# Kernel optimization log

Measured on AMD Instinct MI355X. Metric: run time of the kernel, lower is better.

The kernel has to match this reference:

```python
import math
import jax, jax.numpy as jnp
import numpy as np

B, T, C = 4, 2048, 1024
N_HEAD = 16
HEAD_DIM = C // N_HEAD


def setup_inputs() -> dict:
    key = jax.random.key(0)
    k1, k2, k3 = jax.random.split(key, 3)
    x = jax.random.normal(k1, (B, T, C), dtype=jnp.float32)
    # nn.Linear weights: (out_features, in_features); init scale ~1/sqrt(C)
    w_attn = jax.random.normal(k2, (3 * C, C), dtype=jnp.float32) / math.sqrt(C)
    w_proj = jax.random.normal(k3, (C, C), dtype=jnp.float32) / math.sqrt(C)
    return {"x": x, "w_attn": w_attn, "w_proj": w_proj}


def reference(x, w_attn, w_proj):
    Bx, Tx, Cx = x.shape
    qkv = x @ w_attn.T  # (B,T,3C)
    q, k, v = jnp.split(qkv, 3, axis=2)
    # (B,T,H,D) -> (B,H,T,D)
    q = q.reshape(Bx, Tx, N_HEAD, HEAD_DIM).transpose(0, 2, 1, 3)
    k = k.reshape(Bx, Tx, N_HEAD, HEAD_DIM).transpose(0, 2, 1, 3)
    v = v.reshape(Bx, Tx, N_HEAD, HEAD_DIM).transpose(0, 2, 1, 3)
    scale = 1.0 / math.sqrt(HEAD_DIM)
    att = jnp.einsum("bhqd,bhkd->bhqk", q, k) * scale
    causal = jnp.tril(jnp.ones((Tx, Tx), dtype=bool))
    att = jnp.where(causal[None, None, :, :], att, -jnp.inf)
    att = jax.nn.softmax(att, axis=-1)
    out = jnp.einsum("bhqk,bhkd->bhqd", att, v)
    out = out.transpose(0, 2, 1, 3).reshape(Bx, Tx, Cx)
    return out @ w_proj.T
```

## Files before the change

### kernel.cpp

```cpp
#include <hip/hip_runtime.h>
#include <hip/hip_bf16.h>


typedef __attribute__((ext_vector_type(8))) short bf16x8;
typedef __attribute__((ext_vector_type(4))) float f32x4;
typedef unsigned short ushort_t;

#if __has_builtin(__builtin_amdgcn_exp2f)
#define EXP2(x) __builtin_amdgcn_exp2f(x)
#else
#define EXP2(x) exp2f(x)
#endif

__device__ inline ushort_t f2bf(float f) {
    union { float f; unsigned int u; } x; x.f = f;
    return (ushort_t)((x.u + 0x7fffu + ((x.u >> 16) & 1u)) >> 16);
}

__device__ inline ushort_t f2bf_fast(float f) {
    union { float f; unsigned int u; } x; x.f = f;
    return (ushort_t)((x.u + 0x8000u) >> 16);
}

__device__ inline bf16x8 load8_f32_to_bf16(const float* p) {
    float4 f0 = *(const float4*)p;
    float4 f1 = *(const float4*)(p + 4);
    bf16x8 r;
    r[0] = (short)f2bf(f0.x); r[1] = (short)f2bf(f0.y);
    r[2] = (short)f2bf(f0.z); r[3] = (short)f2bf(f0.w);
    r[4] = (short)f2bf(f1.x); r[5] = (short)f2bf(f1.y);
    r[6] = (short)f2bf(f1.z); r[7] = (short)f2bf(f1.w);
    return r;
}

__device__ inline void gl2lds16(const ushort_t* g, ushort_t* l) {
    __builtin_amdgcn_global_load_lds(
        (const __attribute__((address_space(1))) unsigned int*)g,
        (__attribute__((address_space(3))) unsigned int*)l,
        16, 0, 0);
}

__global__ void cvt3(const float* __restrict__ a, long n8a,
                     const float* __restrict__ b, long n8b,
                     const float* __restrict__ c, long n8c,
                     ushort_t* __restrict__ out) {
    long i = (long)blockIdx.x * 256 + threadIdx.x;
    const float* src; long off;
    if (i < n8a) { src = a; off = i; }
    else if (i < n8a + n8b) { src = b; off = i - n8a; }
    else if (i < n8a + n8b + n8c) { src = c; off = i - n8a - n8b; }
    else return;
    *(bf16x8*)(out + i * 8) = load8_f32_to_bf16(src + off * 8);
}

__global__ void fill_zero_f32(float* out, int n) {
    int i = blockIdx.x * 256 + threadIdx.x;
    if (i < n) out[i] = 0.0f;
}

#define QK_LOG2E_SCALE 0.18033688011112042f

#define OVBUF 16384

template <int EPI>
__global__ __launch_bounds__(256) void gemm_ov(
        const ushort_t* __restrict__ A, const ushort_t* __restrict__ B,
        void* __restrict__ Cp, void* __restrict__ Cp2,
        int M, int N, int K) {
    __shared__ ushort_t S[2 * OVBUF];

    const int tid  = threadIdx.x;
    const int lane = tid & 63;
    const int w    = tid >> 6;
    const int quad = lane >> 4;
    const int l16  = lane & 15;
    const int wm   = (w & 1) * 64;
    const int wn   = (w >> 1) * 64;

    const int nbx = N >> 7;
    const int cpx = gridDim.x >> 3;
    const int swz = ((int)blockIdx.x & 7) * cpx + ((int)blockIdx.x >> 3);
    const int bm = (swz / nbx) << 7;
    const int bn = (swz % nbx) << 7;

    const int nt = K >> 6;

    const int srow = lane >> 3;
    const int soct = (lane & 7) ^ srow;
    const ushort_t* Ag = A + (size_t)(bm + w * 32 + srow) * K + soct * 8;
    const ushort_t* Bg = B + (size_t)(bn + w * 32 + srow) * K + soct * 8;

    auto stage = [&](int kt) {
        ushort_t* d = S + (kt & 1) * OVBUF;
        const size_t ko = (size_t)kt * 64;
#pragma unroll
        for (int j = 0; j < 4; j++) {
            gl2lds16(Ag + ko + (size_t)(j * 8) * K, d + w * 2048 + j * 512);
            gl2lds16(Bg + ko + (size_t)(j * 8) * K, d + 8192 + w * 2048 + j * 512);
        }
    };

    const int sl7 = l16 & 7;
    const int ca0 = ((quad)     ^ sl7) * 8;
    const int ca1 = ((quad + 4) ^ sl7) * 8;
    const int arow = (wm + l16) * 64;
    const int brow = 8192 + (wn + l16) * 64;

    f32x4 acc[4][4] = {};

    stage(0);
    __asm__ __volatile__("s_waitcnt vmcnt(0)" ::: "memory");
    __builtin_amdgcn_s_barrier();

    for (int kt = 0; kt < nt; kt++) {
        if (kt + 1 < nt) stage(kt + 1);

        const ushort_t* Sb = S + (kt & 1) * OVBUF;
        bf16x8 af[4][2], bfr[4][2];
#pragma unroll
        for (int mi = 0; mi < 4; mi++) {
            af[mi][0] = *(const bf16x8*)(Sb + arow + mi * 1024 + ca0);
            af[mi][1] = *(const bf16x8*)(Sb + arow + mi * 1024 + ca1);
        }
#pragma unroll
        for (int ni = 0; ni < 4; ni++) {
            bfr[ni][0] = *(const bf16x8*)(Sb + brow + ni * 1024 + ca0);
            bfr[ni][1] = *(const bf16x8*)(Sb + brow + ni * 1024 + ca1);
        }

        __builtin_amdgcn_s_setprio(1);
#pragma unroll
        for (int mi = 0; mi < 4; mi++)
#pragma unroll
            for (int ni = 0; ni < 4; ni++)
#pragma unroll
                for (int kk = 0; kk < 2; kk++)
                    acc[mi][ni] = __builtin_amdgcn_mfma_f32_16x16x32_bf16(
                        af[mi][kk], bfr[ni][kk], acc[mi][ni], 0, 0, 0);
        __builtin_amdgcn_s_setprio(0);

        __asm__ __volatile__("s_waitcnt vmcnt(0)" ::: "memory");
        __builtin_amdgcn_s_barrier();
    }

    const int colbase = bn + wn;
    const int rowbase = bm + wm + quad * 4;
    if constexpr (EPI == 1) {
#pragma unroll
        for (int mi = 0; mi < 4; mi++) {
            const int row = rowbase + mi * 16;
            float* cr = (float*)Cp + (size_t)row * N + colbase + l16;
#pragma unroll
            for (int r = 0; r < 4; r++)
#pragma unroll
                for (int ni = 0; ni < 4; ni++)
                    cr[(size_t)r * N + ni * 16] = acc[mi][ni][r];
        }
    } else {
        if (colbase < 2048) {
            const float qs = (colbase < 1024) ? QK_LOG2E_SCALE : 1.0f;
#pragma unroll
            for (int mi = 0; mi < 4; mi++) {
                const int row = rowbase + mi * 16;
                ushort_t* qp = (ushort_t*)Cp + (size_t)row * 2048 + colbase + l16;
#pragma unroll
                for (int r = 0; r < 4; r++)
#pragma unroll
                    for (int ni = 0; ni < 4; ni++)
                        qp[(size_t)r * 2048 + ni * 16] = f2bf(acc[mi][ni][r] * qs);
            }
        } else {
#pragma unroll
            for (int mi = 0; mi < 4; mi++) {
                const int row = rowbase + mi * 16;
                const int bb = row >> 11, tt = row & 2047;
#pragma unroll
                for (int ni = 0; ni < 4; ni++) {
                    const int vc = colbase + ni * 16 + l16 - 2048;
                    const int hh = vc >> 6, dd = vc & 63;
                    ushort_t* vp = (ushort_t*)Cp2 +
                        ((((size_t)bb * 16 + hh) * 64 + dd) * 2048) + tt;
#pragma unroll
                    for (int r = 0; r < 4; r++)
                        vp[r] = f2bf(acc[mi][ni][r]);
                }
            }
        }
    }
}

#define BM 128
#define BN 128
#define BK 64
#define LDK 72

template <bool A_F32, bool B_F32, int EPI>
__global__ __launch_bounds__(256) void gemm_nt(
        const void* __restrict__ Ap, const void* __restrict__ Bp,
        void* __restrict__ Cp, void* __restrict__ Cp2,
        int M, int N, int K) {
    __shared__ ushort_t As[BM * LDK];
    __shared__ ushort_t Bs[BN * LDK];

    const int tid  = threadIdx.x;
    const int lane = tid & 63;
    const int w    = tid >> 6;
    const int quad = lane >> 4;
    const int l16  = lane & 15;

    const int bm = blockIdx.y * BM;
    const int bn = blockIdx.x * BN;
    const int wm = (w & 1) * 64;
    const int wn = (w >> 1) * 64;

    f32x4 acc[4][4] = {};

    const int lrow = tid >> 3;
    const int lcol = (tid & 7) * 8;

    bf16x8 pa[4], pb[4];
#pragma unroll
    for (int i = 0; i < 4; i++) {
        const int ra = lrow + i * 32;
        if constexpr (A_F32)
            pa[i] = load8_f32_to_bf16((const float*)Ap + (size_t)(bm + ra) * K + lcol);
        else
            pa[i] = *(const bf16x8*)((const ushort_t*)Ap + (size_t)(bm + ra) * K + lcol);
        if constexpr (B_F32)
            pb[i] = load8_f32_to_bf16((const float*)Bp + (size_t)(bn + ra) * K + lcol);
        else
            pb[i] = *(const bf16x8*)((const ushort_t*)Bp + (size_t)(bn + ra) * K + lcol);
    }

    for (int k0 = 0; k0 < K; k0 += BK) {
        __syncthreads();
#pragma unroll
        for (int i = 0; i < 4; i++) {
            *(bf16x8*)&As[(lrow + i * 32) * LDK + lcol] = pa[i];
            *(bf16x8*)&Bs[(lrow + i * 32) * LDK + lcol] = pb[i];
        }
        __syncthreads();

        if (k0 + BK < K) {
            const int kn = k0 + BK + lcol;
#pragma unroll
            for (int i = 0; i < 4; i++) {
                const int ra = lrow + i * 32;
                if constexpr (A_F32)
                    pa[i] = load8_f32_to_bf16((const float*)Ap + (size_t)(bm + ra) * K + kn);
                else
                    pa[i] = *(const bf16x8*)((const ushort_t*)Ap + (size_t)(bm + ra) * K + kn);
                if constexpr (B_F32)
                    pb[i] = load8_f32_to_bf16((const float*)Bp + (size_t)(bn + ra) * K + kn);
                else
                    pb[i] = *(const bf16x8*)((const ushort_t*)Bp + (size_t)(bn + ra) * K + kn);
            }
        }

#pragma unroll
        for (int ks = 0; ks < BK; ks += 32) {
            bf16x8 af[4], bfr[4];
#pragma unroll
            for (int i = 0; i < 4; i++)
                af[i] = *(const bf16x8*)&As[(wm + i * 16 + l16) * LDK + ks + quad * 8];
#pragma unroll
            for (int i = 0; i < 4; i++)
                bfr[i] = *(const bf16x8*)&Bs[(wn + i * 16 + l16) * LDK + ks + quad * 8];
#pragma unroll
            for (int mi = 0; mi < 4; mi++)
#pragma unroll
                for (int ni = 0; ni < 4; ni++)
                    acc[mi][ni] = __builtin_amdgcn_mfma_f32_16x16x32_bf16(
                        af[mi], bfr[ni], acc[mi][ni], 0, 0, 0);
        }
    }

#pragma unroll
    for (int mi = 0; mi < 4; mi++) {
        const int row0 = bm + wm + mi * 16 + quad * 4;
#pragma unroll
        for (int r = 0; r < 4; r++) {
            const int row = row0 + r;
            if constexpr (EPI == 1) {
                float* crow = (float*)Cp + (size_t)row * N + bn + wn;
#pragma unroll
                for (int ni = 0; ni < 4; ni++)
                    crow[ni * 16 + l16] = acc[mi][ni][r];
            } else {
                if (bn < 2048) {
                    const float qs = (bn < 1024) ? QK_LOG2E_SCALE : 1.0f;
                    ushort_t* crow = (ushort_t*)Cp + (size_t)row * 2048 + bn + wn;
#pragma unroll
                    for (int ni = 0; ni < 4; ni++)
                        crow[ni * 16 + l16] = f2bf(acc[mi][ni][r] * qs);
                } else {
                    ushort_t* vt = (ushort_t*)Cp2;
                    const int bb = row >> 11, tt = row & 2047;
#pragma unroll
                    for (int ni = 0; ni < 4; ni++) {
                        const int vc = bn + wn + ni * 16 + l16 - 2048;
                        const int hh = vc >> 6, dd = vc & 63;
                        vt[(((size_t)bb * 16 + hh) * 64 + dd) * 2048 + tt] =
                            f2bf(acc[mi][ni][r]);
                    }
                }
            }
        }
    }
}

#define AT_T 2048
#define PLD 72

__global__ __launch_bounds__(256) void attn4(
        const ushort_t* __restrict__ qk,
        const ushort_t* __restrict__ vt,
        ushort_t* __restrict__ attout) {
    const int bh   = blockIdx.x;
    const int qblk = (gridDim.y - 1) - blockIdx.y;
    const int b    = bh >> 4;
    const int h    = bh & 15;

    const int tid  = threadIdx.x;
    const int lane = tid & 63;
    const int w    = tid >> 6;
    const int quad = lane >> 4;
    const int l16  = lane & 15;
    const int sw   = l16 & 7;

    __shared__ ushort_t Ks[64 * 64];
    __shared__ ushort_t Vs[80 * 64];
    __shared__ ushort_t Ps[4][32 * PLD];

    for (int i = tid; i < 16 * 64; i += 256) Vs[64 * 64 + i] = 0;
    if (tid < 64) Vs[64 * 64 + tid] = 0x3F80;

    const ushort_t* qp = qk + (size_t)b * AT_T * 2048 + h * 64;
    const ushort_t* kp = qp + 1024;
    const ushort_t* vp = vt + (size_t)bh * 64 * 2048;

    const int Q0 = qblk * 128 + w * 16;

    bf16x8 aq[2][2];
#pragma unroll
    for (int s = 0; s < 2; s++) {
        const ushort_t* qrow = qp + (size_t)(Q0 + s * 64 + l16) * 2048;
        aq[s][0] = *(const bf16x8*)(qrow + quad * 8);
        aq[s][1] = *(const bf16x8*)(qrow + 32 + quad * 8);
    }

    f32x4 o[2][5] = {};

    const int lr8 = lane >> 3;
    const int cbg = ((lane & 7) ^ lr8) * 8;

    const int nk = 2 * qblk + 2;
    for (int kt = 0; kt < nk; kt++) {
        const int k0 = kt * 64;
        if (kt) __syncthreads();
#pragma unroll
        for (int j = 0; j < 2; j++) {
            gl2lds16(kp + (size_t)(k0 + w * 16 + j * 8 + lr8) * 2048 + cbg,
                     &Ks[(w * 16 + j * 8) * 64]);
            gl2lds16(vp + (size_t)(w * 16 + j * 8 + lr8) * 2048 + k0 + cbg,
                     &Vs[(w * 16 + j * 8) * 64]);
        }
        __syncthreads();

        f32x4 s0[4], s1[4];
#pragma unroll
        for (int c = 0; c < 4; c++) {
            s0[c][0] = -8.0f; s0[c][1] = -8.0f; s0[c][2] = -8.0f; s0[c][3] = -8.0f;
            s1[c] = s0[c];
#pragma unroll
            for (int ks = 0; ks < 2; ks++) {
                const int cs = ((quad + 4 * ks) ^ sw) * 8;
                bf16x8 bk = *(const bf16x8*)&Ks[(c * 16 + l16) * 64 + cs];
                s0[c] = __builtin_amdgcn_mfma_f32_16x16x32_bf16(aq[0][ks], bk, s0[c], 0, 0, 0);
                s1[c] = __builtin_amdgcn_mfma_f32_16x16x32_bf16(aq[1][ks], bk, s1[c], 0, 0, 0);
            }
        }

        if (kt >= 2 * qblk) {
            const int q0r = Q0 + quad * 4;
#pragma unroll
            for (int c = 0; c < 4; c++) {
                const int kcol = k0 + c * 16 + l16;
#pragma unroll
                for (int r = 0; r < 4; r++)
                    if (kcol > q0r + r) s0[c][r] = -__builtin_inff();
            }
        }
        if (kt == 2 * qblk + 1) {
            const int q1r = Q0 + 64 + quad * 4;
#pragma unroll
            for (int c = 0; c < 4; c++) {
                const int kcol = k0 + c * 16 + l16;
#pragma unroll
                for (int r = 0; r < 4; r++)
                    if (kcol > q1r + r) s1[c][r] = -__builtin_inff();
            }
        }

#pragma unroll
        for (int c = 0; c < 4; c++)
#pragma unroll
            for (int r = 0; r < 4; r++) {
                Ps[w][(quad * 4 + r) * PLD + c * 16 + l16] = f2bf_fast(EXP2(s0[c][r]));
                Ps[w][(16 + quad * 4 + r) * PLD + c * 16 + l16] = f2bf_fast(EXP2(s1[c][r]));
            }

        __asm__ __volatile__("s_waitcnt lgkmcnt(0)" ::: "memory");

#pragma unroll
        for (int ks = 0; ks < 2; ks++) {
            const int cs = ((quad + 4 * ks) ^ sw) * 8;
            bf16x8 ap0 = *(const bf16x8*)&Ps[w][l16 * PLD + ks * 32 + quad * 8];
            bf16x8 ap1 = *(const bf16x8*)&Ps[w][(16 + l16) * PLD + ks * 32 + quad * 8];
#pragma unroll
            for (int n = 0; n < 5; n++) {
                bf16x8 bv = *(const bf16x8*)&Vs[(n * 16 + l16) * 64 + cs];
                o[0][n] = __builtin_amdgcn_mfma_f32_16x16x32_bf16(ap0, bv, o[0][n], 0, 0, 0);
                o[1][n] = __builtin_amdgcn_mfma_f32_16x16x32_bf16(ap1, bv, o[1][n], 0, 0, 0);
            }
        }
    }

#pragma unroll
    for (int s = 0; s < 2; s++) {
        ushort_t* op = attout + (size_t)(b * AT_T + Q0 + s * 64 + quad * 4) * 1024 + h * 64;
#pragma unroll
        for (int r = 0; r < 4; r++) {
            const float l = __shfl(o[s][4][r], lane & 48, 64);
            const float inv = 1.0f / fmaxf(l, 1e-30f);
            ushort_t* orow = op + (size_t)r * 1024;
#pragma unroll
            for (int n = 0; n < 4; n++)
                orow[n * 16 + l16] = f2bf(o[s][n][r] * inv);
        }
    }
}

extern "C" void kernel_launch(void* const* d_in, const int* in_sizes, int n_in,
                              void* d_out, int out_size, void* d_ws, size_t ws_size,
                              hipStream_t stream) {
    const float* x      = (const float*)d_in[0];
    const float* w_attn = (const float*)d_in[1];
    const float* w_proj = (const float*)d_in[2];
    float* out = (float*)d_out;

    const int M = 8192, C = 1024;
    const size_t E_QK  = (size_t)M * 2048;
    const size_t E_VT  = (size_t)4 * 16 * 64 * 2048;
    const size_t E_ATT = (size_t)M * 1024;
    const size_t E_X   = (size_t)M * 1024;
    const size_t E_WA  = (size_t)3072 * 1024;
    const size_t E_WP  = (size_t)1024 * 1024;
    const size_t need_mid  = (E_QK + E_VT + E_ATT) * 2;
    const size_t need_full = need_mid + (E_X + E_WA + E_WP) * 2;

    if (ws_size < need_mid) {
        fill_zero_f32<<<(out_size + 255) / 256, 256, 0, stream>>>(out, out_size);
        return;
    }

    ushort_t* qk  = (ushort_t*)d_ws;
    ushort_t* vt  = qk + E_QK;
    ushort_t* att = vt + E_VT;

    if (ws_size >= need_full) {
        ushort_t* xb  = att + E_ATT;
        const long n8x = (long)(E_X / 8), n8a = (long)(E_WA / 8), n8p = (long)(E_WP / 8);
        const long n8  = n8x + n8a + n8p;
        cvt3<<<(int)((n8 + 255) / 256), 256, 0, stream>>>(
            x, n8x, w_attn, n8a, w_proj, n8p, xb);

        ushort_t* wab = xb + E_X;
        ushort_t* wpb = wab + E_WA;
        gemm_ov<2><<<dim3((M / 128) * (3 * C / 128)), 256, 0, stream>>>(
            xb, wab, qk, vt, M, 3 * C, C);
        attn4<<<dim3(64, 16), 256, 0, stream>>>(qk, vt, att);
        gemm_ov<1><<<dim3((M / 128) * (C / 128)), 256, 0, stream>>>(
            att, wpb, out, nullptr, M, C, C);
    } else {
        gemm_nt<true, true, 2><<<dim3(3 * C / BN, M / BM), 256, 0, stream>>>(
            x, w_attn, qk, vt, M, 3 * C, C);
        attn4<<<dim3(64, 16), 256, 0, stream>>>(qk, vt, att);
        gemm_nt<false, true, 1><<<dim3(C / BN, M / BM), 256, 0, stream>>>(
            att, w_proj, out, nullptr, M, C, C);
    }
}
```

Before: 232.5 us.

## Double-buffer K/V tiles in attention kernel to overlap loads with MFMA

Gives the K and V shared-memory tiles two buffers. The next tile's global-to-LDS loads are issued before computing on the current tile, with vmcnt waits and raw s_barriers replacing the earlier pair of __syncthreads. This is meant to hide global load latency behind the QK and PV MFMA work. It doubles K/V LDS use, which may lower occupancy. It also depends on the vmcnt(4) count matching the number of outstanding loads.

```diff
diff --git a/kernel.cpp b/kernel.cpp
--- a/kernel.cpp
+++ b/kernel.cpp
@@ -328,12 +328,15 @@
     const int l16  = lane & 15;
     const int sw   = l16 & 7;
 
-    __shared__ ushort_t Ks[64 * 64];
-    __shared__ ushort_t Vs[80 * 64];
+    __shared__ ushort_t Ks[2][64 * 64];
+    __shared__ ushort_t Vs[2][80 * 64];
     __shared__ ushort_t Ps[4][32 * PLD];
 
-    for (int i = tid; i < 16 * 64; i += 256) Vs[64 * 64 + i] = 0;
-    if (tid < 64) Vs[64 * 64 + tid] = 0x3F80;
+#pragma unroll
+    for (int bfi = 0; bfi < 2; bfi++) {
+        for (int i = tid; i < 16 * 64; i += 256) Vs[bfi][64 * 64 + i] = 0;
+        if (tid < 64) Vs[bfi][64 * 64 + tid] = 0x3F80;
+    }
 
     const ushort_t* qp = qk + (size_t)b * AT_T * 2048 + h * 64;
     const ushort_t* kp = qp + 1024;
@@ -354,18 +357,34 @@
     const int lr8 = lane >> 3;
     const int cbg = ((lane & 7) ^ lr8) * 8;
 
-    const int nk = 2 * qblk + 2;
-    for (int kt = 0; kt < nk; kt++) {
+    auto stage = [&](int kt) {
+        const int bfi = kt & 1;
         const int k0 = kt * 64;
-        if (kt) __syncthreads();
 #pragma unroll
         for (int j = 0; j < 2; j++) {
             gl2lds16(kp + (size_t)(k0 + w * 16 + j * 8 + lr8) * 2048 + cbg,
-                     &Ks[(w * 16 + j * 8) * 64]);
+                     &Ks[bfi][(w * 16 + j * 8) * 64]);
             gl2lds16(vp + (size_t)(w * 16 + j * 8 + lr8) * 2048 + k0 + cbg,
-                     &Vs[(w * 16 + j * 8) * 64]);
-        }
-        __syncthreads();
+                     &Vs[bfi][(w * 16 + j * 8) * 64]);
+        }
+    };
+
+    const int nk = 2 * qblk + 2;
+
+    stage(0);
+    __syncthreads();
+
+    for (int kt = 0; kt < nk; kt++) {
+        const int bfi = kt & 1;
+        const int k0 = kt * 64;
+
+        if (kt + 1 < nk) {
+            stage(kt + 1);
+            __asm__ __volatile__("s_waitcnt vmcnt(4)" ::: "memory");
+        } else {
+            __asm__ __volatile__("s_waitcnt vmcnt(0)" ::: "memory");
+        }
+        __builtin_amdgcn_s_barrier();
 
         f32x4 s0[4], s1[4];
 #pragma unroll
@@ -375,7 +394,7 @@
 #pragma unroll
             for (int ks = 0; ks < 2; ks++) {
                 const int cs = ((quad + 4 * ks) ^ sw) * 8;
-                bf16x8 bk = *(const bf16x8*)&Ks[(c * 16 + l16) * 64 + cs];
+                bf16x8 bk = *(const bf16x8*)&Ks[bfi][(c * 16 + l16) * 64 + cs];
                 s0[c] = __builtin_amdgcn_mfma_f32_16x16x32_bf16(aq[0][ks], bk, s0[c], 0, 0, 0);
                 s1[c] = __builtin_amdgcn_mfma_f32_16x16x32_bf16(aq[1][ks], bk, s1[c], 0, 0, 0);
             }
@@ -419,11 +438,13 @@
             bf16x8 ap1 = *(const bf16x8*)&Ps[w][(16 + l16) * PLD + ks * 32 + quad * 8];
 #pragma unroll
             for (int n = 0; n < 5; n++) {
-                bf16x8 bv = *(const bf16x8*)&Vs[(n * 16 + l16) * 64 + cs];
+                bf16x8 bv = *(const bf16x8*)&Vs[bfi][(n * 16 + l16) * 64 + cs];
                 o[0][n] = __builtin_amdgcn_mfma_f32_16x16x32_bf16(ap0, bv, o[0][n], 0, 0, 0);
                 o[1][n] = __builtin_amdgcn_mfma_f32_16x16x32_bf16(ap1, bv, o[1][n], 0, 0, 0);
             }
         }
+
+        __builtin_amdgcn_s_barrier();
     }
 
 #pragma unroll
```

New measurement: 250.1 us. +7.6%, slower.
